# Performance work log

Measured on AMD Instinct MI355X. Metric: run time of the kernel, lower is better.

Reference implementation:

```python
import jax, jax.numpy as jnp
import numpy as np

N_NODES = 100000   # nodes in the sampled subgraph (len(entity))
N_EDGES = 1000000  # edges
DIM = 128          # dim_size
N_REL = 16         # num_relations * 2 (conv is built with doubled relations)
N_ENT = 500000     # num_entities (embedding table rows)


def setup_inputs() -> dict:
    key = jax.random.key(0)
    ks = jax.random.split(key, 9)
    s = 1.0 / np.sqrt(DIM)
    entity = jax.random.randint(ks[0], (N_NODES,), 0, N_ENT)
    edge_index = jax.random.randint(ks[1], (2, N_EDGES), 0, N_NODES)
    edge_type = jax.random.randint(ks[2], (N_EDGES,), 0, N_REL)
    edge_norm = jax.random.normal(ks[3], (N_EDGES,), dtype=jnp.float32)  # unused by the module's math
    emb_table = jax.random.normal(ks[4], (N_ENT, DIM), dtype=jnp.float32)
    W1 = jax.random.normal(ks[5], (N_REL, DIM, DIM), dtype=jnp.float32) * s
    root1 = jax.random.normal(ks[6], (DIM, DIM), dtype=jnp.float32) * s
    W2 = jax.random.normal(ks[7], (N_REL, DIM, DIM), dtype=jnp.float32) * s
    root2 = jax.random.normal(ks[8], (DIM, DIM), dtype=jnp.float32) * s
    return {"entity": entity, "edge_index": edge_index, "edge_type": edge_type,
            "edge_norm": edge_norm, "emb_table": emb_table,
            "W1": W1, "root1": root1, "W2": W2, "root2": root2}


def _rgcn_conv(x, src, dst, edge_type, W_rel, W_root):
    # Relation-routed linear on source features, then scatter-MEAN to dst, plus root linear.
    # Project every node by every relation matrix once (R small), then gather per-edge:
    h_all = jnp.einsum('nd,rdo->rno', x, W_rel)        # [R, N, D]
    msgs = h_all[edge_type, src]                       # [E, D] per-edge messages
    n = x.shape[0]
    agg = jax.ops.segment_sum(msgs, dst, num_segments=n)
    cnt = jax.ops.segment_sum(jnp.ones(src.shape, x.dtype), dst, num_segments=n)
    agg = agg / jnp.maximum(cnt, 1.0)[:, None]         # mean; zero-degree nodes stay 0 (PyG semantics)
    return agg + x @ W_root


def reference(entity, edge_index, edge_type, edge_norm, emb_table, W1, root1, W2, root2):
    src, dst = edge_index[0], edge_index[1]
    x = emb_table[entity]                              # nn.Embedding lookup
    x = jax.nn.relu(_rgcn_conv(x, src, dst, edge_type, W1, root1))
    # dropout is identity in eval mode
    x = _rgcn_conv(x, src, dst, edge_type, W2, root2)
    return x
```

## Files before the change

### kernel.cpp

```cpp
#include <hip/hip_runtime.h>
#include <hip/hip_bf16.h>
#include <stdint.h>

#define D     128
#define DPAD  136
#define TM    64
#define NB    256
#define RMAX  64
#define RS    16
#define NSB   128
#define NST   256

typedef __bf16 bf16_t;
typedef __bf16 bf16x8 __attribute__((ext_vector_type(8)));
typedef float  f32x4  __attribute__((ext_vector_type(4)));


__global__ void deg_kernel(const int* __restrict__ ei, int E, int* __restrict__ cnt) {
    int e = blockIdx.x * blockDim.x + threadIdx.x;
    if (e < E) atomicAdd(&cnt[ei[E + e]], 1);
}

__global__ void inv_kernel(const int* __restrict__ cnt, float* __restrict__ inv, int N) {
    int n = blockIdx.x * blockDim.x + threadIdx.x;
    if (n < N) inv[n] = 1.0f / (float)max(cnt[n], 1);
}

__global__ void hist_kernel(const int* __restrict__ et, int E, int chunk,
                            int R, int* __restrict__ blockhist) {
    __shared__ int h[RMAX];
    int tid = threadIdx.x;
    if (tid < R) h[tid] = 0;
    __syncthreads();
    int start = blockIdx.x * chunk;
    int end   = min(E, start + chunk);
    for (int i = start + tid; i < end; i += blockDim.x)
        atomicAdd(&h[et[i]], 1);
    __syncthreads();
    if (tid < R) blockhist[blockIdx.x * R + tid] = h[tid];
}

__global__ void scan_kernel(int* __restrict__ blockhist, int R,
                            int* __restrict__ blockoff,
                            int* __restrict__ rel_off, int* __restrict__ tile_base,
                            int* __restrict__ tile_rel, int* __restrict__ tile_idx) {
    __shared__ int s_bh[NB * RS];
    __shared__ int tot[RMAX];
    __shared__ int s_off[RMAX + 1], s_tb[RMAX + 1];
    int tid = threadIdx.x;
    const bool staged = (R <= RS);
    if (staged) {
        for (int i = tid; i < NB * R; i += blockDim.x) {
            int b = i / R, r = i - b * R;
            s_bh[r * NB + b] = blockhist[i];
        }
    }
    __syncthreads();
    if (tid < R) {
        int run = 0;
        if (staged) { for (int b = 0; b < NB; b++) run += s_bh[tid * NB + b]; }
        else        { for (int b = 0; b < NB; b++) run += blockhist[b * R + tid]; }
        tot[tid] = run;
    }
    __syncthreads();
    if (tid == 0) {
        int acc = 0, tb = 0;
        for (int r = 0; r < R; r++) {
            s_off[r] = acc; s_tb[r] = tb;
            acc += tot[r];
            tb  += (tot[r] + TM - 1) / TM;
        }
        s_off[R] = acc; s_tb[R] = tb;
    }
    __syncthreads();
    if (tid <= R) {
        rel_off[tid]   = s_off[tid];
        tile_base[tid] = s_tb[tid];
    }
    if (tid < R) {
        int run = s_off[tid];
        for (int b = 0; b < NB; b++) {
            int v = staged ? s_bh[tid * NB + b] : blockhist[b * R + tid];
            blockoff[b * R + tid] = run;
            run += v;
        }
    }
    __syncthreads();
    for (int r = 0; r < R; r++) {
        int nt = s_tb[r + 1] - s_tb[r];
        for (int t = tid; t < nt; t += blockDim.x) {
            tile_rel[s_tb[r] + t] = r;
            tile_idx[s_tb[r] + t] = t;
        }
    }
}

__global__ void scatter2_kernel(const int* __restrict__ ei, const int* __restrict__ et,
                                int E, int chunk, int R,
                                const int* __restrict__ blockoff,
                                int* __restrict__ s_src, int* s_dst, int* relpos) {
    __shared__ int ofs[RMAX];
    int tid = threadIdx.x;
    if (tid < R) ofs[tid] = blockoff[blockIdx.x * R + tid];
    __syncthreads();
    int start = blockIdx.x * chunk;
    int end   = min(E, start + chunk);
    for (int i = start + tid; i < end; i += blockDim.x) {
        int r = et[i];
        int p = atomicAdd(&ofs[r], 1);
        s_src[p] = ei[i];
        if (s_dst) s_dst[p] = ei[E + i];
        if (relpos) relpos[i] = p;
    }
}


__global__ void nsum_kernel(const int* __restrict__ cnt, int N, int chunkN,
                            int* __restrict__ bsum) {
    __shared__ int red[NST];
    int b = blockIdx.x, tid = threadIdx.x;
    int s = b * chunkN, e = min(N, s + chunkN);
    int sum = 0;
    for (int i = s + tid; i < e; i += NST) sum += cnt[i];
    red[tid] = sum;
    __syncthreads();
    for (int off = NST / 2; off > 0; off >>= 1) {
        if (tid < off) red[tid] += red[tid + off];
        __syncthreads();
    }
    if (tid == 0) bsum[b] = red[0];
}

__global__ void nscanB_kernel(int* __restrict__ bsum, int nb) {
    __shared__ int ts[NST];
    int tid = threadIdx.x;
    int v = (tid < nb) ? bsum[tid] : 0;
    ts[tid] = v;
    __syncthreads();
    for (int off = 1; off < NST; off <<= 1) {
        int t = (tid >= off) ? ts[tid - off] : 0;
        __syncthreads();
        ts[tid] += t;
        __syncthreads();
    }
    if (tid < nb) bsum[tid] = ts[tid] - v;
    if (tid == nb - 1) bsum[nb] = ts[tid];
}

__global__ void nwrite_kernel(const int* __restrict__ cnt, int N, int chunkN,
                              const int* __restrict__ bsum,
                              int* __restrict__ dst_off, int* __restrict__ dst_ptr) {
    __shared__ int tile[NST];
    __shared__ int carry;
    int b = blockIdx.x, tid = threadIdx.x;
    int s = b * chunkN, e = min(N, s + chunkN);
    if (tid == 0) carry = bsum[b];
    __syncthreads();
    for (int base = s; base < e; base += NST) {
        int i = base + tid;
        int v = (i < e) ? cnt[i] : 0;
        tile[tid] = v;
        __syncthreads();
        for (int off = 1; off < NST; off <<= 1) {
            int t = (tid >= off) ? tile[tid - off] : 0;
            __syncthreads();
            tile[tid] += t;
            __syncthreads();
        }
        int incl = tile[tid];
        int excl = carry + incl - v;
        if (i < e) { dst_off[i] = excl; dst_ptr[i] = excl; }
        __syncthreads();
        if (tid == 0) carry += tile[NST - 1];
        __syncthreads();
    }
    if (b == 0 && tid == 0) dst_off[N] = bsum[NSB];
}

__global__ void dstclaim_kernel(const int* __restrict__ ei, int E,
                                int* __restrict__ dst_ptr,
                                const int* __restrict__ relpos,
                                int* __restrict__ msgpos) {
    int i = blockIdx.x * blockDim.x + threadIdx.x;
    if (i < E) {
        int p = atomicAdd(&dst_ptr[ei[E + i]], 1);
        msgpos[relpos[i]] = p;
    }
}

__global__ void transpose_kernel(const float* __restrict__ W1, const float* __restrict__ root1,
                                 const float* __restrict__ W2, const float* __restrict__ root2,
                                 int R, bf16_t* __restrict__ Wt) {
    int m = blockIdx.x;
    const float* src;
    if (m < R)            src = W1 + (size_t)m * D * D;
    else if (m < 2 * R)   src = W2 + (size_t)(m - R) * D * D;
    else if (m == 2 * R)  src = root1;
    else                  src = root2;
    bf16_t* dstp = Wt + (size_t)m * D * D;
    for (int i = threadIdx.x; i < D * D; i += blockDim.x) {
        int o = i >> 7, d = i & 127;
        dstp[i] = (bf16_t)src[d * D + o];
    }
}

__global__ void gather_kernel(const int* __restrict__ entity, const float* __restrict__ emb,
                              bf16_t* __restrict__ x, int N) {
    int t = blockIdx.x * blockDim.x + threadIdx.x;
    if (t >= N * 16) return;
    int n = t >> 4, c = t & 15;
    const float4* src = (const float4*)(emb + (size_t)entity[n] * D) + c * 2;
    float4 a = src[0], b = src[1];
    bf16x8 v = { (bf16_t)a.x, (bf16_t)a.y, (bf16_t)a.z, (bf16_t)a.w,
                 (bf16_t)b.x, (bf16_t)b.y, (bf16_t)b.z, (bf16_t)b.w };
    *(bf16x8*)(x + (size_t)t * 8) = v;
}


__global__ __launch_bounds__(256, 3)
void edge_gemm_scatter(const bf16_t* __restrict__ x, const bf16_t* __restrict__ Wt,
                       const int* __restrict__ s_src_g, const int* __restrict__ msgpos,
                       const int* __restrict__ rel_off, const int* __restrict__ tile_base,
                       const int* __restrict__ tile_rel, const int* __restrict__ tile_idx,
                       int R, bf16_t* __restrict__ msgs) {
    __shared__ bf16_t sW[D * DPAD];
    __shared__ bf16_t sA[TM * DPAD];
    __shared__ int   sh_src[TM];
    __shared__ int   sh_slot[TM];

    int tile = blockIdx.x;
    if (tile >= tile_base[R]) return;
    int r = tile_rel[tile];
    int t = tile_idx[tile];
    int base = rel_off[r] + t * TM;
    int cntE = min(TM, rel_off[r + 1] - base);

    int tid = threadIdx.x;
    if (tid < TM) {
        int ok = tid < cntE;
        sh_src[tid]  = ok ? s_src_g[base + tid] : 0;
        sh_slot[tid] = ok ? msgpos[base + tid] : 0;
    }
    const uint4* Wg = (const uint4*)(Wt + (size_t)r * D * D);
    for (int c = tid; c < D * 16; c += 256) {
        int row = c >> 4, col = c & 15;
        *(uint4*)&sW[row * DPAD + col * 8] = Wg[c];
    }
    __syncthreads();
    for (int c = tid; c < TM * 16; c += 256) {
        int row = c >> 4, col = c & 15;
        const uint4* xr = (const uint4*)(x + (size_t)sh_src[row] * D);
        *(uint4*)&sA[row * DPAD + col * 8] = xr[col];
    }
    __syncthreads();

    int lane = tid & 63;
    int w = tid >> 6;
    int m = lane & 15, q = lane >> 4;
    f32x4 acc[4][2];
#pragma unroll
    for (int a = 0; a < 4; a++)
#pragma unroll
        for (int b = 0; b < 2; b++) acc[a][b] = (f32x4){0.f, 0.f, 0.f, 0.f};

#pragma unroll
    for (int k0 = 0; k0 < D; k0 += 32) {
        bf16x8 af[4], bfr[2];
#pragma unroll
        for (int mt = 0; mt < 4; mt++)
            af[mt] = *(const bf16x8*)&sA[(mt * 16 + m) * DPAD + k0 + q * 8];
#pragma unroll
        for (int nt = 0; nt < 2; nt++)
            bfr[nt] = *(const bf16x8*)&sW[(w * 32 + nt * 16 + m) * DPAD + k0 + q * 8];
#pragma unroll
        for (int mt = 0; mt < 4; mt++)
#pragma unroll
            for (int nt = 0; nt < 2; nt++)
                acc[mt][nt] = __builtin_amdgcn_mfma_f32_16x16x32_bf16(af[mt], bfr[nt], acc[mt][nt], 0, 0, 0);
    }

    __syncthreads();
#pragma unroll
    for (int mt = 0; mt < 4; mt++)
#pragma unroll
        for (int i = 0; i < 4; i++) {
            int row = mt * 16 + q * 4 + i;
#pragma unroll
            for (int nt = 0; nt < 2; nt++)
                sA[row * DPAD + w * 32 + nt * 16 + m] = (bf16_t)acc[mt][nt][i];
        }
    __syncthreads();
    for (int c = tid; c < cntE * 16; c += 256) {
        int row = c >> 4, col = c & 15;
        ((uint4*)msgs)[(size_t)sh_slot[row] * 16 + col] = *(uint4*)&sA[row * DPAD + col * 8];
    }
}

__global__ __launch_bounds__(256, 3)
void edge_gemm_atomic(const bf16_t* __restrict__ x, const bf16_t* __restrict__ Wt,
                      const int* __restrict__ s_src_g, const int* __restrict__ s_dst_g,
                      const float* __restrict__ inv_cnt,
                      const int* __restrict__ rel_off, const int* __restrict__ tile_base,
                      const int* __restrict__ tile_rel, const int* __restrict__ tile_idx,
                      int R, float* __restrict__ agg) {
    __shared__ bf16_t sW[D * DPAD];
    __shared__ bf16_t sA[TM * DPAD];
    __shared__ int   sh_src[TM];
    __shared__ int   sh_dst[TM];
    __shared__ float sh_inv[TM];

    int tile = blockIdx.x;
    if (tile >= tile_base[R]) return;
    int r = tile_rel[tile];
    int t = tile_idx[tile];
    int base = rel_off[r] + t * TM;
    int cntE = min(TM, rel_off[r + 1] - base);

    int tid = threadIdx.x;
    if (tid < TM) {
        int ok = tid < cntE;
        int s  = ok ? s_src_g[base + tid] : 0;
        int dd = ok ? s_dst_g[base + tid] : 0;
        sh_src[tid] = s;
        sh_dst[tid] = dd;
        sh_inv[tid] = ok ? inv_cnt[dd] : 0.f;
    }
    const uint4* Wg = (const uint4*)(Wt + (size_t)r * D * D);
    for (int c = tid; c < D * 16; c += 256) {
        int row = c >> 4, col = c & 15;
        *(uint4*)&sW[row * DPAD + col * 8] = Wg[c];
    }
    __syncthreads();
    for (int c = tid; c < TM * 16; c += 256) {
        int row = c >> 4, col = c & 15;
        const uint4* xr = (const uint4*)(x + (size_t)sh_src[row] * D);
        *(uint4*)&sA[row * DPAD + col * 8] = xr[col];
    }
    __syncthreads();

    int lane = tid & 63;
    int w = tid >> 6;
    int m = lane & 15, q = lane >> 4;
    f32x4 acc[4][2];
#pragma unroll
    for (int a = 0; a < 4; a++)
#pragma unroll
        for (int b = 0; b < 2; b++) acc[a][b] = (f32x4){0.f, 0.f, 0.f, 0.f};

#pragma unroll
    for (int k0 = 0; k0 < D; k0 += 32) {
        bf16x8 af[4], bfr[2];
#pragma unroll
        for (int mt = 0; mt < 4; mt++)
            af[mt] = *(const bf16x8*)&sA[(mt * 16 + m) * DPAD + k0 + q * 8];
#pragma unroll
        for (int nt = 0; nt < 2; nt++)
            bfr[nt] = *(const bf16x8*)&sW[(w * 32 + nt * 16 + m) * DPAD + k0 + q * 8];
#pragma unroll
        for (int mt = 0; mt < 4; mt++)
#pragma unroll
            for (int nt = 0; nt < 2; nt++)
                acc[mt][nt] = __builtin_amdgcn_mfma_f32_16x16x32_bf16(af[mt], bfr[nt], acc[mt][nt], 0, 0, 0);
    }

#pragma unroll
    for (int mt = 0; mt < 4; mt++)
#pragma unroll
        for (int i = 0; i < 4; i++) {
            int edge = mt * 16 + q * 4 + i;
            if (edge < cntE) {
                float sc = sh_inv[edge];
                float* ag = agg + (size_t)sh_dst[edge] * D;
#pragma unroll
                for (int nt = 0; nt < 2; nt++) {
                    int o = w * 32 + nt * 16 + m;
                    atomicAdd(&ag[o], acc[mt][nt][i] * sc);
                }
            }
        }
}

__global__ __launch_bounds__(256)
void seg_sum(const bf16_t* __restrict__ msgs, const int* __restrict__ dst_off,
             const float* __restrict__ inv, float* __restrict__ agg, int N) {
    int node = blockIdx.x * 16 + (threadIdx.x >> 4);
    int t = threadIdx.x & 15;
    if (node >= N) return;
    int s = dst_off[node], e = dst_off[node + 1];
    float sum[8] = {0.f, 0.f, 0.f, 0.f, 0.f, 0.f, 0.f, 0.f};
    for (int j = s; j < e; j++) {
        bf16x8 v = *(const bf16x8*)(msgs + (size_t)j * D + t * 8);
#pragma unroll
        for (int k = 0; k < 8; k++) sum[k] += (float)v[k];
    }
    float sc = inv[node];
    float* out = agg + (size_t)node * D + t * 8;
    *(float4*)out       = (float4){sum[0] * sc, sum[1] * sc, sum[2] * sc, sum[3] * sc};
    *(float4*)(out + 4) = (float4){sum[4] * sc, sum[5] * sc, sum[6] * sc, sum[7] * sc};
}

__global__ __launch_bounds__(256, 3)
void root_gemm(const bf16_t* x, const bf16_t* __restrict__ roott,
               const float* __restrict__ agg, bf16_t* out16, float* out32,
               int N, int relu) {
    __shared__ bf16_t sW[D * DPAD];
    __shared__ bf16_t sA[TM * DPAD];
    int tid = threadIdx.x;
    int nbase = blockIdx.x * TM;

    const uint4* Wg = (const uint4*)roott;
    for (int c = tid; c < D * 16; c += 256) {
        int row = c >> 4, col = c & 15;
        *(uint4*)&sW[row * DPAD + col * 8] = Wg[c];
    }
    for (int c = tid; c < TM * 16; c += 256) {
        int row = c >> 4, col = c & 15;
        int n = nbase + row;
        if (n >= N) n = N - 1;
        *(uint4*)&sA[row * DPAD + col * 8] = ((const uint4*)(x + (size_t)n * D))[col];
    }
    __syncthreads();

    int lane = tid & 63;
    int w = tid >> 6;
    int m = lane & 15, q = lane >> 4;
    f32x4 acc[4][2];
#pragma unroll
    for (int a = 0; a < 4; a++)
#pragma unroll
        for (int b = 0; b < 2; b++) acc[a][b] = (f32x4){0.f, 0.f, 0.f, 0.f};

#pragma unroll
    for (int k0 = 0; k0 < D; k0 += 32) {
        bf16x8 af[4], bfr[2];
#pragma unroll
        for (int mt = 0; mt < 4; mt++)
            af[mt] = *(const bf16x8*)&sA[(mt * 16 + m) * DPAD + k0 + q * 8];
#pragma unroll
        for (int nt = 0; nt < 2; nt++)
            bfr[nt] = *(const bf16x8*)&sW[(w * 32 + nt * 16 + m) * DPAD + k0 + q * 8];
#pragma unroll
        for (int mt = 0; mt < 4; mt++)
#pragma unroll
            for (int nt = 0; nt < 2; nt++)
                acc[mt][nt] = __builtin_amdgcn_mfma_f32_16x16x32_bf16(af[mt], bfr[nt], acc[mt][nt], 0, 0, 0);
    }

#pragma unroll
    for (int mt = 0; mt < 4; mt++)
#pragma unroll
        for (int i = 0; i < 4; i++) {
            int row = mt * 16 + q * 4 + i;
            int n = nbase + row;
            if (n < N) {
#pragma unroll
                for (int nt = 0; nt < 2; nt++) {
                    int o = w * 32 + nt * 16 + m;
                    float v = acc[mt][nt][i] + agg[(size_t)n * D + o];
                    if (relu) v = fmaxf(v, 0.f);
                    if (out16) out16[(size_t)n * D + o] = (bf16_t)v;
                    else       out32[(size_t)n * D + o] = v;
                }
            }
        }
}


extern "C" void kernel_launch(void* const* d_in, const int* in_sizes, int n_in,
                              void* d_out, int out_size, void* d_ws, size_t ws_size,
                              hipStream_t stream) {
    const int*   entity = (const int*)d_in[0];
    const int*   ei     = (const int*)d_in[1];
    const int*   et     = (const int*)d_in[2];
    const float* emb    = (const float*)d_in[4];
    const float* W1     = (const float*)d_in[5];
    const float* root1  = (const float*)d_in[6];
    const float* W2     = (const float*)d_in[7];
    const float* root2  = (const float*)d_in[8];

    const int N = in_sizes[0];
    const int E = in_sizes[2];
    const int R = in_sizes[5] / (D * D);

    char* p = (char*)d_ws;
    auto alloc = [&](size_t bytes) -> char* {
        char* q = p; p += (bytes + 255) & ~(size_t)255; return q;
    };
    float*  agg      = (float*)alloc((size_t)N * D * 4);
    bf16_t* x        = (bf16_t*)alloc((size_t)N * D * 2);
    bf16_t* Wt       = (bf16_t*)alloc((size_t)(2 * R + 2) * D * D * 2);
    int*    s_src    = (int*)alloc((size_t)E * 4);
    int*    cnt      = (int*)alloc((size_t)N * 4);
    float*  inv      = (float*)alloc((size_t)N * 4);
    int*    blockhist= (int*)alloc((size_t)NB * R * 4);
    int*    blockoff = (int*)alloc((size_t)NB * R * 4);
    int*    rel_off  = (int*)alloc((size_t)(R + 1) * 4);
    int*    tile_bs  = (int*)alloc((size_t)(R + 1) * 4);
    const int maxtiles = (E + TM - 1) / TM + R;
    int*    tile_rel = (int*)alloc((size_t)maxtiles * 4);
    int*    tile_idx = (int*)alloc((size_t)maxtiles * 4);
    char*   p_common = p;

    bf16_t* msgs    = (bf16_t*)alloc((size_t)E * D * 2);
    int*    relpos  = (int*)alloc((size_t)E * 4);
    int*    msgpos  = (int*)alloc((size_t)E * 4);
    int*    dst_off = (int*)alloc((size_t)(N + 1) * 4);
    int*    dst_ptr = (int*)alloc((size_t)N * 4);
    int*    bsum    = (int*)alloc((size_t)(NSB + 1) * 4);
    bool big = ((size_t)(p - (char*)d_ws) <= ws_size);

    int* s_dst = nullptr;
    if (!big) { p = p_common; s_dst = (int*)alloc((size_t)E * 4); }

    const int chunk = (E + NB - 1) / NB;

    hipMemsetAsync(cnt, 0, (size_t)N * 4, stream);
    deg_kernel<<<(E + 255) / 256, 256, 0, stream>>>(ei, E, cnt);
    inv_kernel<<<(N + 255) / 256, 256, 0, stream>>>(cnt, inv, N);
    hist_kernel<<<NB, 256, 0, stream>>>(et, E, chunk, R, blockhist);
    scan_kernel<<<1, 256, 0, stream>>>(blockhist, R, blockoff, rel_off, tile_bs, tile_rel, tile_idx);
    scatter2_kernel<<<NB, 256, 0, stream>>>(ei, et, E, chunk, R, blockoff,
                                            s_src, big ? nullptr : s_dst, big ? relpos : nullptr);
    transpose_kernel<<<2 * R + 2, 256, 0, stream>>>(W1, root1, W2, root2, R, Wt);
    gather_kernel<<<(N * 16 + 255) / 256, 256, 0, stream>>>(entity, emb, x, N);

    if (big) {
        const int chunkN = (N + NSB - 1) / NSB;
        nsum_kernel<<<NSB, NST, 0, stream>>>(cnt, N, chunkN, bsum);
        nscanB_kernel<<<1, NST, 0, stream>>>(bsum, NSB);
        nwrite_kernel<<<NSB, NST, 0, stream>>>(cnt, N, chunkN, bsum, dst_off, dst_ptr);
        dstclaim_kernel<<<(E + 255) / 256, 256, 0, stream>>>(ei, E, dst_ptr, relpos, msgpos);

        edge_gemm_scatter<<<maxtiles, 256, 0, stream>>>(x, Wt, s_src, msgpos,
                                                        rel_off, tile_bs, tile_rel, tile_idx, R, msgs);
        seg_sum<<<(N + 15) / 16, 256, 0, stream>>>(msgs, dst_off, inv, agg, N);
        root_gemm<<<(N + TM - 1) / TM, 256, 0, stream>>>(x, Wt + (size_t)(2 * R) * D * D, agg,
                                                         x, (float*)nullptr, N, 1);
        edge_gemm_scatter<<<maxtiles, 256, 0, stream>>>(x, Wt + (size_t)R * D * D, s_src, msgpos,
                                                        rel_off, tile_bs, tile_rel, tile_idx, R, msgs);
        seg_sum<<<(N + 15) / 16, 256, 0, stream>>>(msgs, dst_off, inv, agg, N);
        root_gemm<<<(N + TM - 1) / TM, 256, 0, stream>>>(x, Wt + (size_t)(2 * R + 1) * D * D, agg,
                                                         (bf16_t*)nullptr, (float*)d_out, N, 0);
    } else {
        hipMemsetAsync(agg, 0, (size_t)N * D * 4, stream);
        edge_gemm_atomic<<<maxtiles, 256, 0, stream>>>(x, Wt, s_src, s_dst, inv,
                                                       rel_off, tile_bs, tile_rel, tile_idx, R, agg);
        root_gemm<<<(N + TM - 1) / TM, 256, 0, stream>>>(x, Wt + (size_t)(2 * R) * D * D, agg,
                                                         x, (float*)nullptr, N, 1);
        hipMemsetAsync(agg, 0, (size_t)N * D * 4, stream);
        edge_gemm_atomic<<<maxtiles, 256, 0, stream>>>(x, Wt + (size_t)R * D * D, s_src, s_dst, inv,
                                                       rel_off, tile_bs, tile_rel, tile_idx, R, agg);
        root_gemm<<<(N + TM - 1) / TM, 256, 0, stream>>>(x, Wt + (size_t)(2 * R + 1) * D * D, agg,
                                                         (bf16_t*)nullptr, (float*)d_out, N, 0);
    }
}
```

Before: 963.6 us.

## Fuse segment-mean into root GEMM, merge degree count, enlarge edge tiles

The segment-mean aggregation is now computed per 64-node block straight into shared memory and used as the accumulator seed for the root-weight MFMA GEMM, so the fp32 agg buffer is no longer written and re-read for each layer. The degree count moves into the relation-histogram kernel, and the inverse count comes from CSR offsets on the main path, which removes two launches. Edge GEMM tiles grow from 64 to 128 edges, so each relation weight load serves more edges, at the cost of more registers and shared memory and a lower launch-bounds occupancy target.

```diff
diff --git a/kernel.cpp b/kernel.cpp
--- a/kernel.cpp
+++ b/kernel.cpp
@@ -4,40 +4,39 @@
 
 #define D     128
 #define DPAD  136
-#define TM    64
+#define TME   128
 #define NB    256
 #define RMAX  64
 #define RS    16
 #define NSB   128
 #define NST   256
+#define AST   132
 
 typedef __bf16 bf16_t;
 typedef __bf16 bf16x8 __attribute__((ext_vector_type(8)));
 typedef float  f32x4  __attribute__((ext_vector_type(4)));
 
 
-__global__ void deg_kernel(const int* __restrict__ ei, int E, int* __restrict__ cnt) {
-    int e = blockIdx.x * blockDim.x + threadIdx.x;
-    if (e < E) atomicAdd(&cnt[ei[E + e]], 1);
+__global__ void hist_kernel(const int* __restrict__ ei, const int* __restrict__ et,
+                            int E, int chunk, int R,
+                            int* __restrict__ blockhist, int* __restrict__ cnt) {
+    __shared__ int h[RMAX];
+    int tid = threadIdx.x;
+    if (tid < R) h[tid] = 0;
+    __syncthreads();
+    int start = blockIdx.x * chunk;
+    int end   = min(E, start + chunk);
+    for (int i = start + tid; i < end; i += blockDim.x) {
+        atomicAdd(&h[et[i]], 1);
+        atomicAdd(&cnt[ei[E + i]], 1);
+    }
+    __syncthreads();
+    if (tid < R) blockhist[blockIdx.x * R + tid] = h[tid];
 }
 
 __global__ void inv_kernel(const int* __restrict__ cnt, float* __restrict__ inv, int N) {
     int n = blockIdx.x * blockDim.x + threadIdx.x;
     if (n < N) inv[n] = 1.0f / (float)max(cnt[n], 1);
-}
-
-__global__ void hist_kernel(const int* __restrict__ et, int E, int chunk,
-                            int R, int* __restrict__ blockhist) {
-    __shared__ int h[RMAX];
-    int tid = threadIdx.x;
-    if (tid < R) h[tid] = 0;
-    __syncthreads();
-    int start = blockIdx.x * chunk;
-    int end   = min(E, start + chunk);
-    for (int i = start + tid; i < end; i += blockDim.x)
-        atomicAdd(&h[et[i]], 1);
-    __syncthreads();
-    if (tid < R) blockhist[blockIdx.x * R + tid] = h[tid];
 }
 
 __global__ void scan_kernel(int* __restrict__ blockhist, int R,
@@ -68,7 +67,7 @@
         for (int r = 0; r < R; r++) {
             s_off[r] = acc; s_tb[r] = tb;
             acc += tot[r];
-            tb  += (tot[r] + TM - 1) / TM;
+            tb  += (tot[r] + TME - 1) / TME;
         }
         s_off[R] = acc; s_tb[R] = tb;
     }
@@ -217,26 +216,26 @@
 }
 
 
-__global__ __launch_bounds__(256, 3)
+__global__ __launch_bounds__(256, 2)
 void edge_gemm_scatter(const bf16_t* __restrict__ x, const bf16_t* __restrict__ Wt,
                        const int* __restrict__ s_src_g, const int* __restrict__ msgpos,
                        const int* __restrict__ rel_off, const int* __restrict__ tile_base,
                        const int* __restrict__ tile_rel, const int* __restrict__ tile_idx,
                        int R, bf16_t* __restrict__ msgs) {
     __shared__ bf16_t sW[D * DPAD];
-    __shared__ bf16_t sA[TM * DPAD];
-    __shared__ int   sh_src[TM];
-    __shared__ int   sh_slot[TM];
+    __shared__ bf16_t sA[TME * DPAD];
+    __shared__ int   sh_src[TME];
+    __shared__ int   sh_slot[TME];
 
     int tile = blockIdx.x;
     if (tile >= tile_base[R]) return;
     int r = tile_rel[tile];
     int t = tile_idx[tile];
-    int base = rel_off[r] + t * TM;
-    int cntE = min(TM, rel_off[r + 1] - base);
-
-    int tid = threadIdx.x;
-    if (tid < TM) {
+    int base = rel_off[r] + t * TME;
+    int cntE = min(TME, rel_off[r + 1] - base);
+
+    int tid = threadIdx.x;
+    if (tid < TME) {
         int ok = tid < cntE;
         sh_src[tid]  = ok ? s_src_g[base + tid] : 0;
         sh_slot[tid] = ok ? msgpos[base + tid] : 0;
@@ -247,7 +246,7 @@
         *(uint4*)&sW[row * DPAD + col * 8] = Wg[c];
     }
     __syncthreads();
-    for (int c = tid; c < TM * 16; c += 256) {
+    for (int c = tid; c < TME * 16; c += 256) {
         int row = c >> 4, col = c & 15;
         const uint4* xr = (const uint4*)(x + (size_t)sh_src[row] * D);
         *(uint4*)&sA[row * DPAD + col * 8] = xr[col];
@@ -257,23 +256,23 @@
     int lane = tid & 63;
     int w = tid >> 6;
     int m = lane & 15, q = lane >> 4;
-    f32x4 acc[4][2];
-#pragma unroll
-    for (int a = 0; a < 4; a++)
+    f32x4 acc[8][2];
+#pragma unroll
+    for (int a = 0; a < 8; a++)
 #pragma unroll
         for (int b = 0; b < 2; b++) acc[a][b] = (f32x4){0.f, 0.f, 0.f, 0.f};
 
 #pragma unroll
     for (int k0 = 0; k0 < D; k0 += 32) {
-        bf16x8 af[4], bfr[2];
-#pragma unroll
-        for (int mt = 0; mt < 4; mt++)
+        bf16x8 af[8], bfr[2];
+#pragma unroll
+        for (int mt = 0; mt < 8; mt++)
             af[mt] = *(const bf16x8*)&sA[(mt * 16 + m) * DPAD + k0 + q * 8];
 #pragma unroll
         for (int nt = 0; nt < 2; nt++)
             bfr[nt] = *(const bf16x8*)&sW[(w * 32 + nt * 16 + m) * DPAD + k0 + q * 8];
 #pragma unroll
-        for (int mt = 0; mt < 4; mt++)
+        for (int mt = 0; mt < 8; mt++)
 #pragma unroll
             for (int nt = 0; nt < 2; nt++)
                 acc[mt][nt] = __builtin_amdgcn_mfma_f32_16x16x32_bf16(af[mt], bfr[nt], acc[mt][nt], 0, 0, 0);
@@ -281,7 +280,7 @@
 
     __syncthreads();
 #pragma unroll
-    for (int mt = 0; mt < 4; mt++)
+    for (int mt = 0; mt < 8; mt++)
 #pragma unroll
         for (int i = 0; i < 4; i++) {
             int row = mt * 16 + q * 4 + i;
@@ -296,7 +295,7 @@
     }
 }
 
-__global__ __launch_bounds__(256, 3)
+__global__ __launch_bounds__(256, 2)
 void edge_gemm_atomic(const bf16_t* __restrict__ x, const bf16_t* __restrict__ Wt,
                       const int* __restrict__ s_src_g, const int* __restrict__ s_dst_g,
                       const float* __restrict__ inv_cnt,
@@ -304,20 +303,20 @@
                       const int* __restrict__ tile_rel, const int* __restrict__ tile_idx,
                       int R, float* __restrict__ agg) {
     __shared__ bf16_t sW[D * DPAD];
-    __shared__ bf16_t sA[TM * DPAD];
-    __shared__ int   sh_src[TM];
-    __shared__ int   sh_dst[TM];
-    __shared__ float sh_inv[TM];
+    __shared__ bf16_t sA[TME * DPAD];
+    __shared__ int   sh_src[TME];
+    __shared__ int   sh_dst[TME];
+    __shared__ float sh_inv[TME];
 
     int tile = blockIdx.x;
     if (tile >= tile_base[R]) return;
     int r = tile_rel[tile];
     int t = tile_idx[tile];
-    int base = rel_off[r] + t * TM;
-    int cntE = min(TM, rel_off[r + 1] - base);
-
-    int tid = threadIdx.x;
-    if (tid < TM) {
+    int base = rel_off[r] + t * TME;
+    int cntE = min(TME, rel_off[r + 1] - base);
+
+    int tid = threadIdx.x;
+    if (tid < TME) {
         int ok = tid < cntE;
         int s  = ok ? s_src_g[base + tid] : 0;
         int dd = ok ? s_dst_g[base + tid] : 0;
@@ -331,7 +330,7 @@
         *(uint4*)&sW[row * DPAD + col * 8] = Wg[c];
     }
     __syncthreads();
-    for (int c = tid; c < TM * 16; c += 256) {
+    for (int c = tid; c < TME * 16; c += 256) {
         int row = c >> 4, col = c & 15;
         const uint4* xr = (const uint4*)(x + (size_t)sh_src[row] * D);
         *(uint4*)&sA[row * DPAD + col * 8] = xr[col];
@@ -341,30 +340,30 @@
     int lane = tid & 63;
     int w = tid >> 6;
     int m = lane & 15, q = lane >> 4;
-    f32x4 acc[4][2];
-#pragma unroll
-    for (int a = 0; a < 4; a++)
+    f32x4 acc[8][2];
+#pragma unroll
+    for (int a = 0; a < 8; a++)
 #pragma unroll
         for (int b = 0; b < 2; b++) acc[a][b] = (f32x4){0.f, 0.f, 0.f, 0.f};
 
 #pragma unroll
     for (int k0 = 0; k0 < D; k0 += 32) {
-        bf16x8 af[4], bfr[2];
-#pragma unroll
-        for (int mt = 0; mt < 4; mt++)
+        bf16x8 af[8], bfr[2];
+#pragma unroll
+        for (int mt = 0; mt < 8; mt++)
             af[mt] = *(const bf16x8*)&sA[(mt * 16 + m) * DPAD + k0 + q * 8];
 #pragma unroll
         for (int nt = 0; nt < 2; nt++)
             bfr[nt] = *(const bf16x8*)&sW[(w * 32 + nt * 16 + m) * DPAD + k0 + q * 8];
 #pragma unroll
-        for (int mt = 0; mt < 4; mt++)
+        for (int mt = 0; mt < 8; mt++)
 #pragma unroll
             for (int nt = 0; nt < 2; nt++)
                 acc[mt][nt] = __builtin_amdgcn_mfma_f32_16x16x32_bf16(af[mt], bfr[nt], acc[mt][nt], 0, 0, 0);
     }
 
 #pragma unroll
-    for (int mt = 0; mt < 4; mt++)
+    for (int mt = 0; mt < 8; mt++)
 #pragma unroll
         for (int i = 0; i < 4; i++) {
             int edge = mt * 16 + q * 4 + i;
@@ -380,23 +379,98 @@
         }
 }
 
-__global__ __launch_bounds__(256)
-void seg_sum(const bf16_t* __restrict__ msgs, const int* __restrict__ dst_off,
-             const float* __restrict__ inv, float* __restrict__ agg, int N) {
-    int node = blockIdx.x * 16 + (threadIdx.x >> 4);
-    int t = threadIdx.x & 15;
-    if (node >= N) return;
-    int s = dst_off[node], e = dst_off[node + 1];
-    float sum[8] = {0.f, 0.f, 0.f, 0.f, 0.f, 0.f, 0.f, 0.f};
-    for (int j = s; j < e; j++) {
-        bf16x8 v = *(const bf16x8*)(msgs + (size_t)j * D + t * 8);
-#pragma unroll
-        for (int k = 0; k < 8; k++) sum[k] += (float)v[k];
-    }
-    float sc = inv[node];
-    float* out = agg + (size_t)node * D + t * 8;
-    *(float4*)out       = (float4){sum[0] * sc, sum[1] * sc, sum[2] * sc, sum[3] * sc};
-    *(float4*)(out + 4) = (float4){sum[4] * sc, sum[5] * sc, sum[6] * sc, sum[7] * sc};
+__global__ __launch_bounds__(256, 3)
+void seg_root_gemm(const bf16_t* __restrict__ msgs, const int* __restrict__ dst_off,
+                   const bf16_t* __restrict__ x, const bf16_t* __restrict__ roott,
+                   bf16_t* out16, float* out32, int N, int relu) {
+    __shared__ __attribute__((aligned(16))) char pool[(D + 64) * DPAD * 2];
+    __shared__ int s_off[65];
+    float*  aggL = (float*)pool;
+    bf16_t* sW   = (bf16_t*)pool;
+    bf16_t* sA   = (bf16_t*)(pool + (size_t)D * DPAD * 2);
+
+    int tid = threadIdx.x;
+    int nbase = blockIdx.x * 64;
+    if (tid < 65) s_off[tid] = dst_off[min(nbase + tid, N)];
+    __syncthreads();
+
+#pragma unroll
+    for (int pass = 0; pass < 4; pass++) {
+        int local = pass * 16 + (tid >> 4);
+        int t = tid & 15;
+        int s = s_off[local], e = s_off[local + 1];
+        float sum[8] = {0.f, 0.f, 0.f, 0.f, 0.f, 0.f, 0.f, 0.f};
+        for (int j = s; j < e; j++) {
+            bf16x8 v = *(const bf16x8*)(msgs + (size_t)j * D + t * 8);
+#pragma unroll
+            for (int k = 0; k < 8; k++) sum[k] += (float)v[k];
+        }
+        float sc = 1.0f / (float)max(e - s, 1);
+        float* o = aggL + local * AST + t * 8;
+        *(f32x4*)o       = (f32x4){sum[0] * sc, sum[1] * sc, sum[2] * sc, sum[3] * sc};
+        *(f32x4*)(o + 4) = (f32x4){sum[4] * sc, sum[5] * sc, sum[6] * sc, sum[7] * sc};
+    }
+    __syncthreads();
+
+    int lane = tid & 63;
+    int w = tid >> 6;
+    int m = lane & 15, q = lane >> 4;
+    f32x4 acc[4][2];
+#pragma unroll
+    for (int mt = 0; mt < 4; mt++)
+#pragma unroll
+        for (int nt = 0; nt < 2; nt++)
+#pragma unroll
+            for (int i = 0; i < 4; i++)
+                acc[mt][nt][i] = aggL[(mt * 16 + q * 4 + i) * AST + (w * 32 + nt * 16 + m)];
+    __syncthreads();
+
+    const uint4* Wg = (const uint4*)roott;
+    for (int c = tid; c < D * 16; c += 256) {
+        int row = c >> 4, col = c & 15;
+        *(uint4*)&sW[row * DPAD + col * 8] = Wg[c];
+    }
+    for (int c = tid; c < 64 * 16; c += 256) {
+        int row = c >> 4, col = c & 15;
+        int n = nbase + row;
+        if (n >= N) n = N - 1;
+        *(uint4*)&sA[row * DPAD + col * 8] = ((const uint4*)(x + (size_t)n * D))[col];
+    }
+    __syncthreads();
+
+#pragma unroll
+    for (int k0 = 0; k0 < D; k0 += 32) {
+        bf16x8 af[4], bfr[2];
+#pragma unroll
+        for (int mt = 0; mt < 4; mt++)
+            af[mt] = *(const bf16x8*)&sA[(mt * 16 + m) * DPAD + k0 + q * 8];
+#pragma unroll
+        for (int nt = 0; nt < 2; nt++)
+            bfr[nt] = *(const bf16x8*)&sW[(w * 32 + nt * 16 + m) * DPAD + k0 + q * 8];
+#pragma unroll
+        for (int mt = 0; mt < 4; mt++)
+#pragma unroll
+            for (int nt = 0; nt < 2; nt++)
+                acc[mt][nt] = __builtin_amdgcn_mfma_f32_16x16x32_bf16(af[mt], bfr[nt], acc[mt][nt], 0, 0, 0);
+    }
+
+#pragma unroll
+    for (int mt = 0; mt < 4; mt++)
+#pragma unroll
+        for (int i = 0; i < 4; i++) {
+            int row = mt * 16 + q * 4 + i;
+            int n = nbase + row;
+            if (n < N) {
+#pragma unroll
+                for (int nt = 0; nt < 2; nt++) {
+                    int o = w * 32 + nt * 16 + m;
+                    float v = acc[mt][nt][i];
+                    if (relu) v = fmaxf(v, 0.f);
+                    if (out16) out16[(size_t)n * D + o] = (bf16_t)v;
+                    else       out32[(size_t)n * D + o] = v;
+                }
+            }
+        }
 }
 
 __global__ __launch_bounds__(256, 3)
@@ -404,16 +478,16 @@
                const float* __restrict__ agg, bf16_t* out16, float* out32,
                int N, int relu) {
     __shared__ bf16_t sW[D * DPAD];
-    __shared__ bf16_t sA[TM * DPAD];
-    int tid = threadIdx.x;
-    int nbase = blockIdx.x * TM;
+    __shared__ bf16_t sA[64 * DPAD];
+    int tid = threadIdx.x;
+    int nbase = blockIdx.x * 64;
 
     const uint4* Wg = (const uint4*)roott;
     for (int c = tid; c < D * 16; c += 256) {
         int row = c >> 4, col = c & 15;
         *(uint4*)&sW[row * DPAD + col * 8] = Wg[c];
     }
-    for (int c = tid; c < TM * 16; c += 256) {
+    for (int c = tid; c < 64 * 16; c += 256) {
         int row = c >> 4, col = c & 15;
         int n = nbase + row;
         if (n >= N) n = N - 1;
@@ -496,7 +570,7 @@
     int*    blockoff = (int*)alloc((size_t)NB * R * 4);
     int*    rel_off  = (int*)alloc((size_t)(R + 1) * 4);
     int*    tile_bs  = (int*)alloc((size_t)(R + 1) * 4);
-    const int maxtiles = (E + TM - 1) / TM + R;
+    const int maxtiles = (E + TME - 1) / TME + R;
     int*    tile_rel = (int*)alloc((size_t)maxtiles * 4);
     int*    tile_idx = (int*)alloc((size_t)maxtiles * 4);
     char*   p_common = p;
@@ -515,9 +589,7 @@
     const int chunk = (E + NB - 1) / NB;
 
     hipMemsetAsync(cnt, 0, (size_t)N * 4, stream);
-    deg_kernel<<<(E + 255) / 256, 256, 0, stream>>>(ei, E, cnt);
-    inv_kernel<<<(N + 255) / 256, 256, 0, stream>>>(cnt, inv, N);
-    hist_kernel<<<NB, 256, 0, stream>>>(et, E, chunk, R, blockhist);
+    hist_kernel<<<NB, 256, 0, stream>>>(ei, et, E, chunk, R, blockhist, cnt);
     scan_kernel<<<1, 256, 0, stream>>>(blockhist, R, blockoff, rel_off, tile_bs, tile_rel, tile_idx);
     scatter2_kernel<<<NB, 256, 0, stream>>>(ei, et, E, chunk, R, blockoff,
                                             s_src, big ? nullptr : s_dst, big ? relpos : nullptr);
@@ -533,24 +605,25 @@
 
         edge_gemm_scatter<<<maxtiles, 256, 0, stream>>>(x, Wt, s_src, msgpos,
                                                         rel_off, tile_bs, tile_rel, tile_idx, R, msgs);
-        seg_sum<<<(N + 15) / 16, 256, 0, stream>>>(msgs, dst_off, inv, agg, N);
-        root_gemm<<<(N + TM - 1) / TM, 256, 0, stream>>>(x, Wt + (size_t)(2 * R) * D * D, agg,
+        seg_root_gemm<<<(N + 63) / 64, 256, 0, stream>>>(msgs, dst_off, x,
+                                                         Wt + (size_t)(2 * R) * D * D,
                                                          x, (float*)nullptr, N, 1);
         edge_gemm_scatter<<<maxtiles, 256, 0, stream>>>(x, Wt + (size_t)R * D * D, s_src, msgpos,
                                                         rel_off, tile_bs, tile_rel, tile_idx, R, msgs);
-        seg_sum<<<(N + 15) / 16, 256, 0, stream>>>(msgs, dst_off, inv, agg, N);
-        root_gemm<<<(N + TM - 1) / TM, 256, 0, stream>>>(x, Wt + (size_t)(2 * R + 1) * D * D, agg,
+        seg_root_gemm<<<(N + 63) / 64, 256, 0, stream>>>(msgs, dst_off, x,
+                                                         Wt + (size_t)(2 * R + 1) * D * D,
                                                          (bf16_t*)nullptr, (float*)d_out, N, 0);
     } else {
+        inv_kernel<<<(N + 255) / 256, 256, 0, stream>>>(cnt, inv, N);
         hipMemsetAsync(agg, 0, (size_t)N * D * 4, stream);
         edge_gemm_atomic<<<maxtiles, 256, 0, stream>>>(x, Wt, s_src, s_dst, inv,
                                                        rel_off, tile_bs, tile_rel, tile_idx, R, agg);
-        root_gemm<<<(N + TM - 1) / TM, 256, 0, stream>>>(x, Wt + (size_t)(2 * R) * D * D, agg,
-                                                         x, (float*)nullptr, N, 1);
+        root_gemm<<<(N + 63) / 64, 256, 0, stream>>>(x, Wt + (size_t)(2 * R) * D * D, agg,
+                                                     x, (float*)nullptr, N, 1);
         hipMemsetAsync(agg, 0, (size_t)N * D * 4, stream);
         edge_gemm_atomic<<<maxtiles, 256, 0, stream>>>(x, Wt + (size_t)R * D * D, s_src, s_dst, inv,
                                                        rel_off, tile_bs, tile_rel, tile_idx, R, agg);
-        root_gemm<<<(N + TM - 1) / TM, 256, 0, stream>>>(x, Wt + (size_t)(2 * R + 1) * D * D, agg,
-                                                         (bf16_t*)nullptr, (float*)d_out, N, 0);
-    }
-}
+        root_gemm<<<(N + 63) / 64, 256, 0, stream>>>(x, Wt + (size_t)(2 * R + 1) * D * D, agg,
+                                                     (bf16_t*)nullptr, (float*)d_out, N, 0);
+    }
+}
```

After: 953.4 us. About the same (-1.1%).
